# Performance work log

Hardware: AMD Instinct MI355X
Metric: run time of the kernel (lower is better)

## Reference

```python
import jax, jax.numpy as jnp
import numpy as np

DIM = 1024
NUM_HEADS = 16
HEAD_DIM = DIM // NUM_HEADS
BATCH = 4
SEQ = 2048
EPS = 1e-6


def rotate_half(x):
    # interleaved-pair rotation: (..., d) -> view (..., d//2, 2), swap with sign
    x = x.reshape(*x.shape[:-1], -1, 2)
    x1, x2 = jnp.split(x, 2, axis=-1)  # each (..., d//2, 1)
    x = jnp.concatenate([-x2, x1], axis=-1)
    return x.reshape(*x.shape[:-2], -1)


def apply_rope(x, cos, sin):
    # x: [B,S,H,D], cos/sin: [S,D]
    cos = cos[None, :, None, :].astype(x.dtype)
    sin = sin[None, :, None, :].astype(x.dtype)
    return x * cos + rotate_half(x) * sin


def rms_norm(x, w):
    var = jnp.mean(jnp.square(x), axis=-1, keepdims=True)
    return x * jax.lax.rsqrt(var + EPS) * w


def setup_inputs() -> dict:
    key = jax.random.key(0)
    ks = jax.random.split(key, 8)
    s = 0.02
    return {
        "x": jax.random.normal(ks[0], (BATCH, SEQ, DIM), jnp.float32),
        "rope_cos": jnp.cos(jnp.arange(SEQ, dtype=jnp.float32)[:, None] *
                            (1.0 / (10000.0 ** (jnp.repeat(jnp.arange(HEAD_DIM // 2, dtype=jnp.float32), 2) * 2 / HEAD_DIM)))[None, :]),
        "rope_sin": jnp.sin(jnp.arange(SEQ, dtype=jnp.float32)[:, None] *
                            (1.0 / (10000.0 ** (jnp.repeat(jnp.arange(HEAD_DIM // 2, dtype=jnp.float32), 2) * 2 / HEAD_DIM)))[None, :]),
        "qkv_w": jax.random.normal(ks[1], (3 * DIM, DIM), jnp.float32) * s,
        "qkv_b": jax.random.normal(ks[2], (3 * DIM,), jnp.float32) * s,
        "proj_w": jax.random.normal(ks[3], (DIM, DIM), jnp.float32) * s,
        "proj_b": jax.random.normal(ks[4], (DIM,), jnp.float32) * s,
        "q_norm_w": jnp.ones((HEAD_DIM,), jnp.float32),
        "k_norm_w": jnp.ones((HEAD_DIM,), jnp.float32),
    }


def reference(x, rope_cos, rope_sin, qkv_w, qkv_b, proj_w, proj_b, q_norm_w, k_norm_w):
    B, S, C = x.shape
    H, D = NUM_HEADS, HEAD_DIM
    qkv = x @ qkv_w.T + qkv_b                      # [B,S,3C]
    qkv = qkv.reshape(B, S, 3, H, D)
    q, k, v = qkv[:, :, 0], qkv[:, :, 1], qkv[:, :, 2]  # [B,S,H,D]
    q = apply_rope(rms_norm(q, q_norm_w), rope_cos, rope_sin)
    k = apply_rope(rms_norm(k, k_norm_w), rope_cos, rope_sin)
    scale = 1.0 / np.sqrt(D).astype(np.float32)
    attn = jnp.einsum('bqhd,bkhd->bhqk', q.astype(jnp.float32), k.astype(jnp.float32))
    attn = jax.nn.softmax(attn * scale, axis=-1).astype(x.dtype)
    out = jnp.einsum('bhqk,bkhd->bqhd', attn, v).reshape(B, S, C)
    return out @ proj_w.T + proj_b
```

## Files before the change

### kernel.cpp

```cpp
#include <hip/hip_runtime.h>
#include <math.h>
#include <type_traits>

#define DIM 1024
#define NH 16
#define HD 64
#define BATCH 4
#define SEQ 2048
#define EPS 1e-6f

typedef __attribute__((ext_vector_type(8))) short short8;
typedef __attribute__((ext_vector_type(4))) short short4v;
typedef __attribute__((ext_vector_type(4))) float float4v;

__device__ inline unsigned short f2bf(float f) {
    unsigned u = __float_as_uint(f);
    u += 0x7FFF + ((u >> 16) & 1);
    return (unsigned short)(u >> 16);
}
__device__ inline float bf2f(unsigned short b) {
    return __uint_as_float(((unsigned)b) << 16);
}
__device__ inline unsigned pk2bf(float lo, float hi) {
    unsigned ul = __float_as_uint(lo) + 0x8000u;
    unsigned uh = __float_as_uint(hi) + 0x8000u;
    return __builtin_amdgcn_perm(uh, ul, 0x07060302u);
}

#if __has_builtin(__builtin_amdgcn_exp2f)
#define EXP2F(x) __builtin_amdgcn_exp2f(x)
#else
#define EXP2F(x) exp2f(x)
#endif

#if __has_builtin(__builtin_amdgcn_mfma_f32_16x16x16bf16_1k)
__device__ inline float4v mfma16(short4v a, short4v b, float4v c) {
    return __builtin_amdgcn_mfma_f32_16x16x16bf16_1k(a, b, c, 0, 0, 0);
}
#elif __has_builtin(__builtin_amdgcn_mfma_f32_16x16x16_bf16)
__device__ inline float4v mfma16(short4v a, short4v b, float4v c) {
    return __builtin_amdgcn_mfma_f32_16x16x16_bf16(a, b, c, 0, 0, 0);
}
#else
__device__ inline float4v mfma16(short4v a, short4v b, float4v c) {
    asm volatile("v_mfma_f32_16x16x16_bf16 %0, %1, %2, %0\n\ts_nop 4"
                 : "+v"(c) : "v"(a), "v"(b));
    return c;
}
#endif

#define GLDS16(gp, lp) __builtin_amdgcn_global_load_lds( \
    (const __attribute__((address_space(1))) void*)(gp), \
    (__attribute__((address_space(3))) void*)(lp), 16, 0, 0)

__global__ __launch_bounds__(256) void prep_all(
    const float* __restrict__ x, const float* __restrict__ qkv_w,
    const float* __restrict__ proj_w,
    const float* __restrict__ cos_t, const float* __restrict__ sin_t,
    unsigned short* __restrict__ xb, unsigned short* __restrict__ qkvwb,
    unsigned short* __restrict__ projwb, unsigned* __restrict__ csP)
{
    const int bid = blockIdx.x;
    if (bid < 8192) {
        int i = bid * 256 + threadIdx.x;
        float4 f = ((const float4*)x)[i];
        ushort4 o;
        o.x = f2bf(f.x); o.y = f2bf(f.y); o.z = f2bf(f.z); o.w = f2bf(f.w);
        ((ushort4*)xb)[i] = o;
    } else if (bid < 8192 + 3072) {
        const int rn = bid - 8192;
        int ro = rn;
        if (rn < 2048) {
            const int head = rn >> 6, c = rn & 63, j = c >> 4, cl = c & 15;
            ro = (head << 6) + ((j & 1) + 2 * cl + 32 * (j >> 1));
        }
        float4 f = ((const float4*)(qkv_w + (long)ro * DIM))[threadIdx.x];
        ushort4 o;
        o.x = f2bf(f.x); o.y = f2bf(f.y); o.z = f2bf(f.z); o.w = f2bf(f.w);
        ((ushort4*)(qkvwb + (long)rn * DIM))[threadIdx.x] = o;
    } else if (bid < 8192 + 3072 + 1024) {
        int i = (bid - 11264) * 256 + threadIdx.x;
        float4 f = ((const float4*)proj_w)[i];
        ushort4 o;
        o.x = f2bf(f.x); o.y = f2bf(f.y); o.z = f2bf(f.z); o.w = f2bf(f.w);
        ((ushort4*)projwb)[i] = o;
    } else {
        int i = (bid - 12288) * 256 + threadIdx.x;
        int a = i >> 11, s = i & 2047;
        float c = cos_t[s * 64 + 2 * a], sn = sin_t[s * 64 + 2 * a];
        csP[a * SEQ + s] = ((unsigned)f2bf(sn) << 16) | f2bf(c);
    }
}

__global__ __launch_bounds__(256) void gemm_qkv_fused(
    const unsigned short* __restrict__ A, const unsigned short* __restrict__ W,
    const float* __restrict__ bias, const unsigned* __restrict__ csP,
    const float* __restrict__ qw, const float* __restrict__ kw,
    unsigned short* __restrict__ q, unsigned short* __restrict__ k,
    unsigned short* __restrict__ vt)
{
    __shared__ __align__(16) unsigned short As[128 * 32];
    __shared__ __align__(16) unsigned short Bs[128 * 32];

    const int t    = threadIdx.x;
    const int lane = t & 63;
    const int w    = t >> 6;
    const int row0 = blockIdx.y * 128;
    const int col0 = blockIdx.x * 128;
    const int wr   = (w & 1) * 64;
    const int wc   = (w >> 1) * 64;
    const int cl   = lane & 15;
    const int quad = lane >> 4;

    float4v acc[4][4];
#pragma unroll
    for (int i = 0; i < 4; ++i)
#pragma unroll
        for (int j = 0; j < 4; ++j) acc[i][j] = (float4v){0.f, 0.f, 0.f, 0.f};

    const int off1 = t * 16, off2 = 4096 + t * 16;
    const int r1 = off1 >> 6, c1 = off1 & 63;
    const int r2 = off2 >> 6, c2 = off2 & 63;
    const char* Ab = (const char*)A + (long)row0 * DIM * 2;
    const char* Wb = (const char*)W + (long)col0 * DIM * 2;
    const long  ks = DIM * 2;

    for (int k0 = 0; k0 < DIM; k0 += 32) {
        const long kb = (long)k0 * 2;
        GLDS16(Ab + (long)r1 * ks + kb + c1, (char*)As + off1);
        GLDS16(Ab + (long)r2 * ks + kb + c2, (char*)As + off2);
        GLDS16(Wb + (long)r1 * ks + kb + c1, (char*)Bs + off1);
        GLDS16(Wb + (long)r2 * ks + kb + c2, (char*)Bs + off2);
        __syncthreads();

        short8 af[4], bfr[4];
#pragma unroll
        for (int i = 0; i < 4; ++i)
            af[i] = *(const short8*)&As[(wr + i * 16 + cl) * 32 + quad * 8];
#pragma unroll
        for (int j = 0; j < 4; ++j)
            bfr[j] = *(const short8*)&Bs[(wc + j * 16 + cl) * 32 + quad * 8];
#pragma unroll
        for (int i = 0; i < 4; ++i)
#pragma unroll
            for (int j = 0; j < 4; ++j)
                acc[i][j] = __builtin_amdgcn_mfma_f32_16x16x32_bf16(af[i], bfr[j], acc[i][j], 0, 0, 0);
        __syncthreads();
    }

    const int gcol  = col0 + wc;
    const int b     = row0 >> 11;
    const int srow0 = (row0 & 2047) + wr;

    if (gcol < 2 * DIM) {
        const bool isq = (gcol < DIM);
        const int  h   = (isq ? gcol : gcol - DIM) >> 6;
        const float* nw = isq ? qw : kw;
        const float scale = isq ? 0.180336880f : 1.0f;
        unsigned short* dst = (isq ? q : k) + (long)(b * NH + h) * SEQ * 64;

        float bjv[4];
#pragma unroll
        for (int j = 0; j < 4; ++j)
            bjv[j] = bias[gcol + (j & 1) + 2 * cl + 32 * (j >> 1)];
#pragma unroll
        for (int i = 0; i < 4; ++i)
#pragma unroll
            for (int j = 0; j < 4; ++j)
#pragma unroll
                for (int r = 0; r < 4; ++r) acc[i][j][r] += bjv[j];

        float rinv[4][4];
#pragma unroll
        for (int i = 0; i < 4; ++i)
#pragma unroll
            for (int r = 0; r < 4; ++r) {
                float ss = acc[i][0][r] * acc[i][0][r];
                ss = fmaf(acc[i][1][r], acc[i][1][r], ss);
                ss = fmaf(acc[i][2][r], acc[i][2][r], ss);
                ss = fmaf(acc[i][3][r], acc[i][3][r], ss);
                ss += __shfl_xor(ss, 1, 64);
                ss += __shfl_xor(ss, 2, 64);
                ss += __shfl_xor(ss, 4, 64);
                ss += __shfl_xor(ss, 8, 64);
                rinv[i][r] = rsqrtf(ss * (1.f / 64.f) + EPS) * scale;
            }

        const float nwe[2] = { nw[2 * cl],     nw[32 + 2 * cl] };
        const float nwo[2] = { nw[2 * cl + 1], nw[33 + 2 * cl] };

#pragma unroll
        for (int i = 0; i < 4; ++i) {
            const int sb = srow0 + i * 16 + quad * 4;
#pragma unroll
            for (int jp = 0; jp < 2; ++jp) {
                uint4 cs4 = *(const uint4*)(csP + (long)(jp * 16 + cl) * SEQ + sb);
#pragma unroll
                for (int r = 0; r < 4; ++r) {
                    float g  = rinv[i][r];
                    float xe = acc[i][2 * jp][r]     * g * nwe[jp];
                    float xo = acc[i][2 * jp + 1][r] * g * nwo[jp];
                    unsigned u = (r == 0) ? cs4.x : (r == 1) ? cs4.y : (r == 2) ? cs4.z : cs4.w;
                    float c  = bf2f((unsigned short)(u & 0xffff));
                    float sn = bf2f((unsigned short)(u >> 16));
                    float oe = fmaf(xe, c, -(xo * sn));
                    float oo = fmaf(xo, c,   xe * sn);
                    *(unsigned*)(dst + (long)(sb + r) * 64 + jp * 32 + 2 * cl) = pk2bf(oe, oo);
                }
            }
        }
    } else {
        const int h = (gcol - 2 * DIM) >> 6;
        float bjv[4];
#pragma unroll
        for (int j = 0; j < 4; ++j) bjv[j] = bias[gcol + j * 16 + cl];
        unsigned short* vdst = vt + (long)(b * NH + h) * SEQ * 64
                                  + (long)(srow0 >> 6) * 4096;
#pragma unroll
        for (int j = 0; j < 4; ++j)
#pragma unroll
            for (int ip = 0; ip < 2; ++ip) {
                const int i0 = 2 * ip;
                uint4 st;
                st.x = pk2bf(acc[i0][j][0] + bjv[j],     acc[i0][j][1] + bjv[j]);
                st.y = pk2bf(acc[i0][j][2] + bjv[j],     acc[i0][j][3] + bjv[j]);
                st.z = pk2bf(acc[i0 + 1][j][0] + bjv[j], acc[i0 + 1][j][1] + bjv[j]);
                st.w = pk2bf(acc[i0 + 1][j][2] + bjv[j], acc[i0 + 1][j][3] + bjv[j]);
                *(uint4*)(vdst + (j * 2 + ip) * 512 + lane * 8) = st;
            }
    }
}

__global__ __launch_bounds__(256) void gemm_proj(
    const unsigned short* __restrict__ A, const unsigned short* __restrict__ W,
    const float* __restrict__ bias, float* __restrict__ C)
{
    __shared__ __align__(16) unsigned short As[128 * 32];
    __shared__ __align__(16) unsigned short Bs[128 * 32];

    const int t    = threadIdx.x;
    const int lane = t & 63;
    const int w    = t >> 6;
    const int row0 = blockIdx.y * 128;
    const int col0 = blockIdx.x * 128;
    const int wr   = (w & 1) * 64;
    const int wc   = (w >> 1) * 64;

    float4v acc[4][4];
#pragma unroll
    for (int i = 0; i < 4; ++i)
#pragma unroll
        for (int j = 0; j < 4; ++j) acc[i][j] = (float4v){0.f, 0.f, 0.f, 0.f};

    const int off1 = t * 16, off2 = 4096 + t * 16;
    const int r1 = off1 >> 6, c1 = off1 & 63;
    const int r2 = off2 >> 6, c2 = off2 & 63;
    const char* Ab = (const char*)A + (long)row0 * DIM * 2;
    const char* Wb = (const char*)W + (long)col0 * DIM * 2;
    const long  ks = DIM * 2;

    for (int k0 = 0; k0 < DIM; k0 += 32) {
        const long kb = (long)k0 * 2;
        GLDS16(Ab + (long)r1 * ks + kb + c1, (char*)As + off1);
        GLDS16(Ab + (long)r2 * ks + kb + c2, (char*)As + off2);
        GLDS16(Wb + (long)r1 * ks + kb + c1, (char*)Bs + off1);
        GLDS16(Wb + (long)r2 * ks + kb + c2, (char*)Bs + off2);
        __syncthreads();

        short8 af[4], bfr[4];
#pragma unroll
        for (int i = 0; i < 4; ++i)
            af[i] = *(const short8*)&As[(wr + i * 16 + (lane & 15)) * 32 + (lane >> 4) * 8];
#pragma unroll
        for (int j = 0; j < 4; ++j)
            bfr[j] = *(const short8*)&Bs[(wc + j * 16 + (lane & 15)) * 32 + (lane >> 4) * 8];
#pragma unroll
        for (int i = 0; i < 4; ++i)
#pragma unroll
            for (int j = 0; j < 4; ++j)
                acc[i][j] = __builtin_amdgcn_mfma_f32_16x16x32_bf16(af[i], bfr[j], acc[i][j], 0, 0, 0);
        __syncthreads();
    }

    const int qd = lane >> 4, cl = lane & 15;
#pragma unroll
    for (int j = 0; j < 4; ++j) {
        const int col = col0 + wc + j * 16 + cl;
        const float bj = bias[col];
#pragma unroll
        for (int i = 0; i < 4; ++i) {
            const long rr = row0 + wr + i * 16 + qd * 4;
#pragma unroll
            for (int r = 0; r < 4; ++r)
                C[(rr + r) * (long)DIM + col] = acc[i][j][r] + bj;
        }
    }
}

__global__ __launch_bounds__(256) void flash_mfma(
    const unsigned short* __restrict__ q, const unsigned short* __restrict__ k,
    const unsigned short* __restrict__ vt, unsigned short* __restrict__ out)
{
    __shared__ __align__(16) unsigned short Ks[2][64 * 32];
    __shared__ __align__(16) unsigned short Vts[64 * 64];

    const int t    = threadIdx.x;
    const int lane = t & 63;
    const int w    = t >> 6;
    const int bh   = blockIdx.y;
    const int b    = bh >> 4;
    const int h    = bh & 15;
    const int q0   = blockIdx.x * 128;
    const int cl   = lane & 15;
    const int quad = lane >> 4;

    const char* qb  = (const char*)(q  + (long)bh * SEQ * 64);
    const char* kb  = (const char*)(k  + (long)bh * SEQ * 64);
    const char* vtb = (const char*)(vt + (long)bh * SEQ * 64);

    short8 aq[2][2];
#pragma unroll
    for (int qg = 0; qg < 2; ++qg)
#pragma unroll
        for (int hf = 0; hf < 2; ++hf)
            aq[qg][hf] = *(const short8*)(qb +
                (long)(q0 + w * 32 + qg * 16 + cl) * 128 + hf * 64 + quad * 16);

    const short4v ones = (short4v){(short)0x3F80, (short)0x3F80,
                                   (short)0x3F80, (short)0x3F80};

    float4v o[2][4], o4[2];
#pragma unroll
    for (int qg = 0; qg < 2; ++qg) {
        o4[qg] = (float4v){0.f, 0.f, 0.f, 0.f};
#pragma unroll
        for (int i = 0; i < 4; ++i) o[qg][i] = (float4v){0.f, 0.f, 0.f, 0.f};
    }

    const int soff = t * 16, srow = soff >> 6, scb = soff & 63;

    for (int kt = 0; kt < SEQ / 64; ++kt) {
#pragma unroll
        for (int hf = 0; hf < 2; ++hf)
            GLDS16(kb + (long)(kt * 64 + srow) * 128 + hf * 64 + scb, (char*)Ks[hf] + soff);
        GLDS16(vtb + (long)kt * 8192 + t * 16,        (char*)Vts + t * 16);
        GLDS16(vtb + (long)kt * 8192 + 4096 + t * 16, (char*)Vts + 4096 + t * 16);
        __syncthreads();

        short4v pa[2][4];
#pragma unroll
        for (int j = 0; j < 4; ++j) {
            short8 a0 = *(const short8*)&Ks[0][(j * 16 + cl) * 32 + quad * 8];
            short8 a1 = *(const short8*)&Ks[1][(j * 16 + cl) * 32 + quad * 8];
#pragma unroll
            for (int qg = 0; qg < 2; ++qg) {
                float4v z = (float4v){0.f, 0.f, 0.f, 0.f};
                z = __builtin_amdgcn_mfma_f32_16x16x32_bf16(a0, aq[qg][0], z, 0, 0, 0);
                float4v s = __builtin_amdgcn_mfma_f32_16x16x32_bf16(a1, aq[qg][1], z, 0, 0, 0);
                float p0 = EXP2F(s[0]), p1 = EXP2F(s[1]);
                float p2 = EXP2F(s[2]), p3 = EXP2F(s[3]);
                unsigned lo = pk2bf(p0, p1), hi = pk2bf(p2, p3);
                pa[qg][j] = __builtin_bit_cast(short4v, ((unsigned long long)hi << 32) | lo);
                o4[qg] = mfma16(ones, pa[qg][j], o4[qg]);
            }
        }

#pragma unroll
        for (int fi = 0; fi < 4; ++fi) {
#pragma unroll
            for (int fjp = 0; fjp < 2; ++fjp) {
                short8 vv = *(const short8*)&Vts[(fi * 2 + fjp) * 512 + lane * 8];
                short4v va = __builtin_shufflevector(vv, vv, 0, 1, 2, 3);
                short4v vb = __builtin_shufflevector(vv, vv, 4, 5, 6, 7);
#pragma unroll
                for (int qg = 0; qg < 2; ++qg) {
                    o[qg][fi] = mfma16(va, pa[qg][2 * fjp],     o[qg][fi]);
                    o[qg][fi] = mfma16(vb, pa[qg][2 * fjp + 1], o[qg][fi]);
                }
            }
        }
        __syncthreads();
    }

#pragma unroll
    for (int qg = 0; qg < 2; ++qg) {
        const float inv = 1.f / o4[qg][0];
        unsigned short* orow = out + ((long)b * SEQ + q0 + w * 32 + qg * 16 + cl) * DIM + h * 64;
#pragma unroll
        for (int i = 0; i < 4; ++i) {
            unsigned lo = pk2bf(o[qg][i][0] * inv, o[qg][i][1] * inv);
            unsigned hi = pk2bf(o[qg][i][2] * inv, o[qg][i][3] * inv);
            ushort4 st = __builtin_bit_cast(ushort4, ((unsigned long long)hi << 32) | lo);
            *(ushort4*)(orow + i * 16 + quad * 4) = st;
        }
    }
}

extern "C" void kernel_launch(void* const* d_in, const int* in_sizes, int n_in,
                              void* d_out, int out_size, void* d_ws, size_t ws_size,
                              hipStream_t stream)
{
    const float* x        = (const float*)d_in[0];
    const float* rope_cos = (const float*)d_in[1];
    const float* rope_sin = (const float*)d_in[2];
    const float* qkv_w    = (const float*)d_in[3];
    const float* qkv_b    = (const float*)d_in[4];
    const float* proj_w   = (const float*)d_in[5];
    const float* proj_b   = (const float*)d_in[6];
    const float* q_norm_w = (const float*)d_in[7];
    const float* k_norm_w = (const float*)d_in[8];
    float* outp = (float*)d_out;

    const int M = BATCH * SEQ;
    char* p = (char*)d_ws;
    unsigned short* xb    = (unsigned short*)p; p += (long)M * DIM * 2;
    unsigned short* qkvwb = (unsigned short*)p; p += (long)3 * DIM * DIM * 2;
    unsigned short* projwb= (unsigned short*)p; p += (long)DIM * DIM * 2;
    unsigned short* qb    = (unsigned short*)p; p += (long)M * DIM * 2;
    unsigned short* kbuf  = (unsigned short*)p; p += (long)M * DIM * 2;
    unsigned short* vtb   = (unsigned short*)p; p += (long)M * DIM * 2;
    unsigned short* attno = (unsigned short*)p; p += (long)M * DIM * 2;
    unsigned*       csP   = (unsigned*)p;       p += (long)32 * SEQ * 4;

    prep_all<<<dim3(12544), 256, 0, stream>>>(
        x, qkv_w, proj_w, rope_cos, rope_sin, xb, qkvwb, projwb, csP);

    gemm_qkv_fused<<<dim3(3 * DIM / 128, M / 128), 256, 0, stream>>>(
        xb, qkvwb, qkv_b, csP, q_norm_w, k_norm_w, qb, kbuf, vtb);

    flash_mfma<<<dim3(SEQ / 128, BATCH * NH), 256, 0, stream>>>(qb, kbuf, vtb, attno);

    gemm_proj<<<dim3(DIM / 128, M / 128), 256, 0, stream>>>(
        attno, projwb, proj_b, outp);
}
```

Baseline: 299.4 us.

## Double-buffer K/V tiles in flash attention to overlap loads with MFMA

Splits the flash-attention shared-memory tiles into two K and two V^T buffers and unrolls the KV loop by two. The next tile's global-to-LDS loads are issued before computing on the current tile, so load latency can hide behind the QK, exp and PV MFMA work. This removes the load-then-wait stall at the top of each iteration. In exchange, LDS use per block doubles, which may reduce occupancy, and the macro-based unroll increases code size.

```diff
diff --git a/kernel.cpp b/kernel.cpp
--- a/kernel.cpp
+++ b/kernel.cpp
@@ -301,8 +301,10 @@
     const unsigned short* __restrict__ q, const unsigned short* __restrict__ k,
     const unsigned short* __restrict__ vt, unsigned short* __restrict__ out)
 {
-    __shared__ __align__(16) unsigned short Ks[2][64 * 32];
-    __shared__ __align__(16) unsigned short Vts[64 * 64];
+    __shared__ __align__(16) unsigned short Ks0[2][64 * 32];
+    __shared__ __align__(16) unsigned short Ks1[2][64 * 32];
+    __shared__ __align__(16) unsigned short Vt0[64 * 64];
+    __shared__ __align__(16) unsigned short Vt1[64 * 64];
 
     const int t    = threadIdx.x;
     const int lane = t & 63;
@@ -339,48 +341,62 @@
 
     const int soff = t * 16, srow = soff >> 6, scb = soff & 63;
 
-    for (int kt = 0; kt < SEQ / 64; ++kt) {
-#pragma unroll
-        for (int hf = 0; hf < 2; ++hf)
-            GLDS16(kb + (long)(kt * 64 + srow) * 128 + hf * 64 + scb, (char*)Ks[hf] + soff);
-        GLDS16(vtb + (long)kt * 8192 + t * 16,        (char*)Vts + t * 16);
-        GLDS16(vtb + (long)kt * 8192 + 4096 + t * 16, (char*)Vts + 4096 + t * 16);
-        __syncthreads();
-
-        short4v pa[2][4];
-#pragma unroll
-        for (int j = 0; j < 4; ++j) {
-            short8 a0 = *(const short8*)&Ks[0][(j * 16 + cl) * 32 + quad * 8];
-            short8 a1 = *(const short8*)&Ks[1][(j * 16 + cl) * 32 + quad * 8];
-#pragma unroll
-            for (int qg = 0; qg < 2; ++qg) {
-                float4v z = (float4v){0.f, 0.f, 0.f, 0.f};
-                z = __builtin_amdgcn_mfma_f32_16x16x32_bf16(a0, aq[qg][0], z, 0, 0, 0);
-                float4v s = __builtin_amdgcn_mfma_f32_16x16x32_bf16(a1, aq[qg][1], z, 0, 0, 0);
-                float p0 = EXP2F(s[0]), p1 = EXP2F(s[1]);
-                float p2 = EXP2F(s[2]), p3 = EXP2F(s[3]);
-                unsigned lo = pk2bf(p0, p1), hi = pk2bf(p2, p3);
-                pa[qg][j] = __builtin_bit_cast(short4v, ((unsigned long long)hi << 32) | lo);
-                o4[qg] = mfma16(ones, pa[qg][j], o4[qg]);
-            }
-        }
-
-#pragma unroll
-        for (int fi = 0; fi < 4; ++fi) {
-#pragma unroll
-            for (int fjp = 0; fjp < 2; ++fjp) {
-                short8 vv = *(const short8*)&Vts[(fi * 2 + fjp) * 512 + lane * 8];
-                short4v va = __builtin_shufflevector(vv, vv, 0, 1, 2, 3);
-                short4v vb = __builtin_shufflevector(vv, vv, 4, 5, 6, 7);
-#pragma unroll
-                for (int qg = 0; qg < 2; ++qg) {
-                    o[qg][fi] = mfma16(va, pa[qg][2 * fjp],     o[qg][fi]);
-                    o[qg][fi] = mfma16(vb, pa[qg][2 * fjp + 1], o[qg][fi]);
-                }
-            }
-        }
-        __syncthreads();
-    }
+#define FLASH_STAGE(ktt, KBUF, VBUF) do {                                        \
+    GLDS16(kb + (long)((ktt) * 64 + srow) * 128 +      scb, (char*)KBUF[0] + soff); \
+    GLDS16(kb + (long)((ktt) * 64 + srow) * 128 + 64 + scb, (char*)KBUF[1] + soff); \
+    GLDS16(vtb + (long)(ktt) * 8192 +        t * 16, (char*)VBUF + t * 16);         \
+    GLDS16(vtb + (long)(ktt) * 8192 + 4096 + t * 16, (char*)VBUF + 4096 + t * 16);  \
+} while (0)
+
+#define FLASH_COMPUTE(KBUF, VBUF) do {                                           \
+    short4v pa[2][4];                                                            \
+    _Pragma("unroll")                                                            \
+    for (int j = 0; j < 4; ++j) {                                                \
+        short8 a0 = *(const short8*)&KBUF[0][(j * 16 + cl) * 32 + quad * 8];     \
+        short8 a1 = *(const short8*)&KBUF[1][(j * 16 + cl) * 32 + quad * 8];     \
+        _Pragma("unroll")                                                        \
+        for (int qg = 0; qg < 2; ++qg) {                                         \
+            float4v z = (float4v){0.f, 0.f, 0.f, 0.f};                           \
+            z = __builtin_amdgcn_mfma_f32_16x16x32_bf16(a0, aq[qg][0], z, 0, 0, 0); \
+            float4v s = __builtin_amdgcn_mfma_f32_16x16x32_bf16(a1, aq[qg][1], z, 0, 0, 0); \
+            float p0 = EXP2F(s[0]), p1 = EXP2F(s[1]);                            \
+            float p2 = EXP2F(s[2]), p3 = EXP2F(s[3]);                            \
+            unsigned lo = pk2bf(p0, p1), hi = pk2bf(p2, p3);                     \
+            pa[qg][j] = __builtin_bit_cast(short4v, ((unsigned long long)hi << 32) | lo); \
+            o4[qg] = mfma16(ones, pa[qg][j], o4[qg]);                            \
+        }                                                                        \
+    }                                                                            \
+    _Pragma("unroll")                                                            \
+    for (int fi = 0; fi < 4; ++fi) {                                             \
+        _Pragma("unroll")                                                        \
+        for (int fjp = 0; fjp < 2; ++fjp) {                                      \
+            short8 vv = *(const short8*)&VBUF[(fi * 2 + fjp) * 512 + lane * 8];  \
+            short4v va = __builtin_shufflevector(vv, vv, 0, 1, 2, 3);            \
+            short4v vb = __builtin_shufflevector(vv, vv, 4, 5, 6, 7);            \
+            _Pragma("unroll")                                                    \
+            for (int qg = 0; qg < 2; ++qg) {                                     \
+                o[qg][fi] = mfma16(va, pa[qg][2 * fjp],     o[qg][fi]);          \
+                o[qg][fi] = mfma16(vb, pa[qg][2 * fjp + 1], o[qg][fi]);          \
+            }                                                                    \
+        }                                                                        \
+    }                                                                            \
+} while (0)
+
+    FLASH_STAGE(0, Ks0, Vt0);
+
+    for (int kt = 0; kt < SEQ / 64; kt += 2) {
+        __syncthreads();
+        FLASH_STAGE(kt + 1, Ks1, Vt1);
+        FLASH_COMPUTE(Ks0, Vt0);
+
+        __syncthreads();
+        if (kt + 2 < SEQ / 64)
+            FLASH_STAGE(kt + 2, Ks0, Vt0);
+        FLASH_COMPUTE(Ks1, Vt1);
+    }
+
+#undef FLASH_STAGE
+#undef FLASH_COMPUTE
 
 #pragma unroll
     for (int qg = 0; qg < 2; ++qg) {
```

New measurement: 302.7 us. About the same (+1.1%).

## Split flash attention over two KV halves with a separate combine kernel

Applied to the files above, without the earlier changes.

Adds a z grid dimension so each attention block processes only half of the key/value sequence. Each block writes unnormalized bf16 partial outputs and partial row sums, and a new combine kernel adds the two halves, normalizes, and scatters into the attention output layout. The goal is more parallelism and shorter per-block loops, at the cost of extra global traffic for the partials, a second launch, and extra bf16 rounding of the partial sums.

```diff
diff --git a/kernel.cpp b/kernel.cpp
--- a/kernel.cpp
+++ b/kernel.cpp
@@ -299,7 +299,8 @@
 
 __global__ __launch_bounds__(256) void flash_mfma(
     const unsigned short* __restrict__ q, const unsigned short* __restrict__ k,
-    const unsigned short* __restrict__ vt, unsigned short* __restrict__ out)
+    const unsigned short* __restrict__ vt,
+    unsigned short* __restrict__ opart, float* __restrict__ lpart)
 {
     __shared__ __align__(16) unsigned short Ks[2][64 * 32];
     __shared__ __align__(16) unsigned short Vts[64 * 64];
@@ -308,8 +309,7 @@
     const int lane = t & 63;
     const int w    = t >> 6;
     const int bh   = blockIdx.y;
-    const int b    = bh >> 4;
-    const int h    = bh & 15;
+    const int z    = blockIdx.z;
     const int q0   = blockIdx.x * 128;
     const int cl   = lane & 15;
     const int quad = lane >> 4;
@@ -338,8 +338,9 @@
     }
 
     const int soff = t * 16, srow = soff >> 6, scb = soff & 63;
-
-    for (int kt = 0; kt < SEQ / 64; ++kt) {
+    const int kt0 = z * (SEQ / 128);
+
+    for (int kt = kt0; kt < kt0 + SEQ / 128; ++kt) {
 #pragma unroll
         for (int hf = 0; hf < 2; ++hf)
             GLDS16(kb + (long)(kt * 64 + srow) * 128 + hf * 64 + scb, (char*)Ks[hf] + soff);
@@ -354,9 +355,9 @@
             short8 a1 = *(const short8*)&Ks[1][(j * 16 + cl) * 32 + quad * 8];
 #pragma unroll
             for (int qg = 0; qg < 2; ++qg) {
-                float4v z = (float4v){0.f, 0.f, 0.f, 0.f};
-                z = __builtin_amdgcn_mfma_f32_16x16x32_bf16(a0, aq[qg][0], z, 0, 0, 0);
-                float4v s = __builtin_amdgcn_mfma_f32_16x16x32_bf16(a1, aq[qg][1], z, 0, 0, 0);
+                float4v zz = (float4v){0.f, 0.f, 0.f, 0.f};
+                zz = __builtin_amdgcn_mfma_f32_16x16x32_bf16(a0, aq[qg][0], zz, 0, 0, 0);
+                float4v s = __builtin_amdgcn_mfma_f32_16x16x32_bf16(a1, aq[qg][1], zz, 0, 0, 0);
                 float p0 = EXP2F(s[0]), p1 = EXP2F(s[1]);
                 float p2 = EXP2F(s[2]), p3 = EXP2F(s[3]);
                 unsigned lo = pk2bf(p0, p1), hi = pk2bf(p2, p3);
@@ -384,16 +385,49 @@
 
 #pragma unroll
     for (int qg = 0; qg < 2; ++qg) {
-        const float inv = 1.f / o4[qg][0];
-        unsigned short* orow = out + ((long)b * SEQ + q0 + w * 32 + qg * 16 + cl) * DIM + h * 64;
+        const int  row  = q0 + w * 32 + qg * 16 + cl;
+        const long rbase = ((long)z * (BATCH * NH) + bh) * SEQ + row;
+        unsigned short* orow = opart + rbase * 64;
 #pragma unroll
         for (int i = 0; i < 4; ++i) {
-            unsigned lo = pk2bf(o[qg][i][0] * inv, o[qg][i][1] * inv);
-            unsigned hi = pk2bf(o[qg][i][2] * inv, o[qg][i][3] * inv);
+            unsigned lo = pk2bf(o[qg][i][0], o[qg][i][1]);
+            unsigned hi = pk2bf(o[qg][i][2], o[qg][i][3]);
             ushort4 st = __builtin_bit_cast(ushort4, ((unsigned long long)hi << 32) | lo);
             *(ushort4*)(orow + i * 16 + quad * 4) = st;
         }
-    }
+        if (quad == 0) lpart[rbase] = o4[qg][0];
+    }
+}
+
+__global__ __launch_bounds__(256) void combine_halves(
+    const unsigned short* __restrict__ opart, const float* __restrict__ lpart,
+    unsigned short* __restrict__ attno)
+{
+    const long HALF = (long)BATCH * NH * SEQ;
+    const int idx = blockIdx.x * 256 + threadIdx.x;
+    const int d8  = idx & 7;
+    const long row = (long)(idx >> 3);
+
+    const float inv = 1.f / (lpart[row] + lpart[HALF + row]);
+
+    const uint4 a = *(const uint4*)(opart + row * 64 + d8 * 8);
+    const uint4 c = *(const uint4*)(opart + (HALF + row) * 64 + d8 * 8);
+
+    unsigned res[4];
+    const unsigned av[4] = {a.x, a.y, a.z, a.w};
+    const unsigned cv[4] = {c.x, c.y, c.z, c.w};
+#pragma unroll
+    for (int m = 0; m < 4; ++m) {
+        float lo = bf2f((unsigned short)(av[m] & 0xffff)) + bf2f((unsigned short)(cv[m] & 0xffff));
+        float hi = bf2f((unsigned short)(av[m] >> 16))    + bf2f((unsigned short)(cv[m] >> 16));
+        res[m] = pk2bf(lo * inv, hi * inv);
+    }
+
+    const int bh = (int)(row >> 11);
+    const int s  = (int)(row & 2047);
+    const int b  = bh >> 4, h = bh & 15;
+    uint4 st; st.x = res[0]; st.y = res[1]; st.z = res[2]; st.w = res[3];
+    *(uint4*)(attno + ((long)(b * SEQ + s)) * DIM + h * 64 + d8 * 8) = st;
 }
 
 extern "C" void kernel_launch(void* const* d_in, const int* in_sizes, int n_in,
@@ -421,6 +455,8 @@
     unsigned short* vtb   = (unsigned short*)p; p += (long)M * DIM * 2;
     unsigned short* attno = (unsigned short*)p; p += (long)M * DIM * 2;
     unsigned*       csP   = (unsigned*)p;       p += (long)32 * SEQ * 4;
+    unsigned short* opart = (unsigned short*)p; p += (long)2 * M * DIM * 2;
+    float*          lpart = (float*)p;          p += (long)2 * BATCH * NH * SEQ * 4;
 
     prep_all<<<dim3(12544), 256, 0, stream>>>(
         x, qkv_w, proj_w, rope_cos, rope_sin, xb, qkvwb, projwb, csP);
@@ -428,7 +464,11 @@
     gemm_qkv_fused<<<dim3(3 * DIM / 128, M / 128), 256, 0, stream>>>(
         xb, qkvwb, qkv_b, csP, q_norm_w, k_norm_w, qb, kbuf, vtb);
 
-    flash_mfma<<<dim3(SEQ / 128, BATCH * NH), 256, 0, stream>>>(qb, kbuf, vtb, attno);
+    flash_mfma<<<dim3(SEQ / 128, BATCH * NH, 2), 256, 0, stream>>>(
+        qb, kbuf, vtb, opart, lpart);
+
+    combine_halves<<<dim3((BATCH * NH * SEQ * 8) / 256), 256, 0, stream>>>(
+        opart, lpart, attno);
 
     gemm_proj<<<dim3(DIM / 128, M / 128), 256, 0, stream>>>(
         attno, projwb, proj_b, outp);
```

Result: slower. 318.7 us (+6.4%).
